# Performance work log

Measured on AMD Instinct MI355X. Metric: run time of the kernel, lower is better.

Reference implementation:

```python
import jax, jax.numpy as jnp
import numpy as np

N, E, G = 50000, 800000, 64
IN_NODE, OUT_NODE, IN_EDGE = 16, 20, 16
HID_E, N_ACT, HID_C = 64, 8, 256
BN_EPS = 1e-5


def setup_inputs() -> dict:
    key = jax.random.key(0)
    ks = jax.random.split(key, 12)
    def w(i, shape, scale=0.05):
        return jax.random.normal(ks[i], shape, jnp.float32) * scale
    return {
        "x": jax.random.normal(ks[0], (N, IN_NODE), jnp.float32),
        "edge_attr": jax.random.normal(ks[1], (E, IN_EDGE), jnp.float32),
        "a": jax.random.normal(ks[2], (G, N_ACT), jnp.float32),
        "edge_index": jax.random.randint(ks[3], (2, E), 0, N),
        "batch": jnp.sort(jax.random.randint(ks[4], (N,), 0, G)),
        # edge-conditioning MLP: Lin(16,64) -> BN(64) -> ReLU -> Lin(64, 16*20)
        "W1": w(5, (IN_EDGE, HID_E)), "b1": jnp.zeros((HID_E,), jnp.float32),
        "gamma": jnp.ones((HID_E,), jnp.float32), "beta": jnp.zeros((HID_E,), jnp.float32),
        "W2": w(6, (HID_E, IN_NODE * OUT_NODE)), "b2": jnp.zeros((IN_NODE * OUT_NODE,), jnp.float32),
        # NNConv root weight + bias
        "root_w": w(7, (IN_NODE, OUT_NODE)), "bias": jnp.zeros((OUT_NODE,), jnp.float32),
        # critic head: Lin(20+8,256) -> ReLU -> Lin(256,1)
        "Wc1": w(8, (OUT_NODE + N_ACT, HID_C)), "bc1": jnp.zeros((HID_C,), jnp.float32),
        "Wc2": w(9, (HID_C, 1)), "bc2": jnp.zeros((1,), jnp.float32),
    }


def reference(x, edge_attr, a, W1, b1, gamma, beta, W2, b2, root_w, bias,
              Wc1, bc1, Wc2, bc2, edge_index, batch):
    # edge-conditioning MLP (BatchNorm in training mode: batch stats over edges)
    h = edge_attr @ W1 + b1                              # [E, 64]
    mu = jnp.mean(h, axis=0)
    var = jnp.mean(jnp.square(h - mu), axis=0)           # biased var, as BN fwd
    h = (h - mu) * jax.lax.rsqrt(var + BN_EPS) * gamma + beta
    h = jax.nn.relu(h)
    w_e = (h @ W2 + b2).reshape(E, IN_NODE, OUT_NODE)    # per-edge weight matrix

    src, dst = edge_index[0], edge_index[1]
    msg = jnp.einsum('ei,eio->eo', x[src], w_e)          # gather + per-edge matvec [E, 20]
    aggr = jax.ops.segment_sum(msg, dst, num_segments=N) # scatter-add (NNConv aggr='add')
    out = x @ root_w + aggr + bias                       # [N, 20]

    # global mean pool over graphs
    sums = jax.ops.segment_sum(out, batch, num_segments=G)            # [G, 20]
    cnt = jax.ops.segment_sum(jnp.ones((N, 1), out.dtype), batch, num_segments=G)
    pooled = sums / jnp.maximum(cnt, 1.0)

    z = jnp.concatenate([pooled, a], axis=1)             # [G, 28]
    z = jax.nn.relu(z @ Wc1 + bc1)
    return z @ Wc2 + bc2                                 # [G, 1]
```

## Files before the change

### kernel.cpp

```cpp
#include <hip/hip_runtime.h>


#define E_EDGES   800000
#define N_NODES   50000
#define G_GRAPHS  64
#define EDGE_GRID 3072
#define NGROUPS   50000
#define GSTRIDE   768
#define NSUP      256
#define STAT_GRID 512
#define QSCALE    131072.0f
#define QINV      (1.0f / 131072.0f)

typedef _Float16 f16x2 __attribute__((ext_vector_type(2)));
typedef _Float16 f16x8 __attribute__((ext_vector_type(8)));
typedef __fp16   fp16x2 __attribute__((ext_vector_type(2)));
typedef float    f32x4 __attribute__((ext_vector_type(4)));
typedef unsigned u32x4 __attribute__((ext_vector_type(4)));

union H2U { f16x2 h; unsigned u; };
union F8U { f16x8 v; f16x2 h2[4]; u32x4 u4; };

__device__ __forceinline__ f16x2 pkrtz(float a, float b) {
  fp16x2 r = __builtin_amdgcn_cvt_pkrtz(a, b);
  return __builtin_bit_cast(f16x2, r);
}

__global__ __launch_bounds__(256) void setup_kernel(
    const float* __restrict__ W2, const float* __restrict__ b2,
    const float* __restrict__ W1, const float* __restrict__ x,
    const float* __restrict__ ea, unsigned* __restrict__ Bbuf,
    unsigned* __restrict__ Bw1, unsigned* __restrict__ xh,
    float* __restrict__ gstatsT)
{
  __shared__ float red[4][272];
  const int b = blockIdx.x, tid = threadIdx.x;
  if (b < STAT_GRID) {
    int lane = tid & 63, wave = tid >> 6;
    int nl = lane & 15, q = lane >> 4;
    int gw = b * 4 + wave;
    f32x4 acc = (f32x4){0.f, 0.f, 0.f, 0.f};
    float ms = 0.f;
    for (int c0 = gw; c0 < E_EDGES / 32; c0 += STAT_GRID * 4) {
      const float* p = ea + (size_t)(c0 * 32 + q * 8) * 16 + nl;
      float v0 = p[0],  v1 = p[16], v2 = p[32], v3 = p[48];
      float v4 = p[64], v5 = p[80], v6 = p[96], v7 = p[112];
      ms += (v0 + v1) + (v2 + v3) + (v4 + v5) + (v6 + v7);
      F8U av;
      av.h2[0] = pkrtz(v0, v1); av.h2[1] = pkrtz(v2, v3);
      av.h2[2] = pkrtz(v4, v5); av.h2[3] = pkrtz(v6, v7);
      acc = __builtin_amdgcn_mfma_f32_16x16x32_f16(av.v, av.v, acc, 0, 0, 0);
    }
    ms += __shfl_xor(ms, 16, 64);
    ms += __shfl_xor(ms, 32, 64);
#pragma unroll
    for (int r = 0; r < 4; ++r) red[wave][(q * 4 + r) * 16 + nl] = acc[r];
    if (q == 0) red[wave][256 + nl] = ms;
    __syncthreads();
    for (int v = tid; v < 272; v += 256)
      gstatsT[(size_t)v * STAT_GRID + b] =
          red[0][v] + red[1][v] + red[2][v] + red[3][v];
  } else if (b < STAT_GRID + 70) {
    int idx = (b - STAT_GRID) * 256 + tid;
    if (idx < 33 * 512) {
      int r = idx & 3, lane = (idx >> 2) & 63, nt = (idx >> 8) & 1,
          s = idx >> 9;
      int q = lane >> 4, nl = lane & 15, n = nt * 16 + nl;
      float v0 = 0.f, v1 = 0.f;
      if (n < 20) {
        if (s < 32) {
          int K0 = s * 32 + q * 8 + 2 * r;
          v0 = W2[(K0 >> 4) * 320 + (K0 & 15) * 20 + n];
          v1 = W2[((K0 + 1) >> 4) * 320 + ((K0 + 1) & 15) * 20 + n];
        } else if (q < 2) {
          int i0 = q * 8 + 2 * r;
          v0 = b2[i0 * 20 + n];
          v1 = b2[(i0 + 1) * 20 + n];
        }
      }
      H2U pk; pk.h = pkrtz(v0, v1);
      Bbuf[idx] = pk.u;
    } else {
      int idx2 = idx - 33 * 512;
      int r = idx2 & 3, lane = (idx2 >> 2) & 63, nt = idx2 >> 8;
      int q = lane >> 4, nl = lane & 15, n = nt * 16 + nl;
      int k0 = q * 8 + 2 * r;
      float v0 = (k0 < 16)     ? W1[k0 * 64 + n]       : 0.f;
      float v1 = (k0 + 1 < 16) ? W1[(k0 + 1) * 64 + n] : 0.f;
      H2U pk; pk.h = pkrtz(v0, v1);
      Bw1[idx2] = pk.u;
    }
  } else {
    int i = (b - STAT_GRID - 70) * 256 + tid;
    if (i < N_NODES * 8) {
      H2U pk; pk.h = pkrtz(x[2 * i], x[2 * i + 1]);
      xh[i] = pk.u;
    }
  }
}

__global__ __launch_bounds__(256) void mid_kernel(
    const float* __restrict__ gstatsT, const float* __restrict__ W1,
    const float* __restrict__ b1, const float* __restrict__ gamma,
    const float* __restrict__ beta, const float* __restrict__ x,
    const int* __restrict__ batch, float* __restrict__ sc,
    float* __restrict__ sh, float* __restrict__ sumx,
    float* __restrict__ cntf)
{
  const int t = threadIdx.x;
  if (blockIdx.x == G_GRAPHS) {
    __shared__ float S[272];
    for (int v = t; v < 272; v += 256) {
      const float* p = gstatsT + (size_t)v * STAT_GRID;
      float s = 0.f;
      for (int bb = 0; bb < STAT_GRID; ++bb) s += p[bb];
      S[v] = s;
    }
    __syncthreads();
    if (t < 64) {
      float w[16];
#pragma unroll
      for (int j = 0; j < 16; ++j) w[j] = W1[j * 64 + t];
      const float invE = 1.0f / (float)E_EDGES;
      float mw = 0.f;
#pragma unroll
      for (int j = 0; j < 16; ++j) mw += S[256 + j] * w[j];
      mw *= invE;
      float qf = 0.f;
      for (int j = 0; j < 16; ++j) {
        float tt = 0.f;
#pragma unroll
        for (int j2 = 0; j2 < 16; ++j2) tt += S[j * 16 + j2] * w[j2];
        qf += w[j] * tt;
      }
      qf *= invE;
      float b = b1[t];
      float meanH = mw + b;
      float eh2 = qf + 2.f * b * mw + b * b;
      float var = eh2 - meanH * meanH;
      float s = gamma[t] * rsqrtf(var + 1e-5f);
      sc[t] = s;
      sh[t] = beta[t] + (b - meanH) * s;
    }
  } else {
    int g = blockIdx.x;
    __shared__ int se[2];
    if (t < 2) {
      int key = g + t;
      int lo = 0, hi = N_NODES;
      while (lo < hi) {
        int mid = (lo + hi) >> 1;
        if (batch[mid] < key) lo = mid + 1; else hi = mid;
      }
      se[t] = lo;
    }
    __syncthreads();
    int start = se[0], end = se[1];
    int c = t & 15, rr = t >> 4;
    float s = 0.f;
    for (int n = start + rr; n < end; n += 16) s += x[(size_t)n * 16 + c];
    __shared__ float red[256];
    red[t] = s;
    __syncthreads();
#pragma unroll
    for (int st = 128; st >= 16; st >>= 1) {
      if (t < st) red[t] += red[t + st];
      __syncthreads();
    }
    if (t < 16) sumx[g * 16 + t] = red[t];
    if (t == 0) cntf[g] = (float)(end - start);
  }
}

__global__ __launch_bounds__(64, 3) void edge_kernel(
    const unsigned* __restrict__ xh, const float* __restrict__ ea,
    const int* __restrict__ ei, const int* __restrict__ batch,
    const float* __restrict__ sc, const float* __restrict__ sh,
    const unsigned* __restrict__ Bbuf, const unsigned* __restrict__ Bw1v,
    int* __restrict__ gpartI)
{
  __shared__ unsigned hh[320];
  __shared__ int gacc[1280];
  const int lane = threadIdx.x;
  const int nl = lane & 15, q = lane >> 4;
  const int s = blockIdx.x;
  const int kq = (s >> 3) & 3;
  const int sgroup = ((s >> 5) << 3) | (s & 7);
  const int* srcp = ei;
  const int* dstp = ei + E_EDGES;

  for (int v = lane; v < 1280; v += 64) gacc[v] = 0;

  F8U bb[8][2];
#pragma unroll
  for (int sl = 0; sl < 8; ++sl)
#pragma unroll
    for (int nt = 0; nt < 2; ++nt)
      bb[sl][nt].u4 =
          ((const u32x4*)Bbuf)[((kq * 8 + sl) * 2 + nt) * 64 + lane];
  F8U bx[2];
  if (kq == 3) {
    bx[0].u4 = ((const u32x4*)Bbuf)[64 * 64 + lane];
    bx[1].u4 = ((const u32x4*)Bbuf)[65 * 64 + lane];
  } else {
    bx[0].u4 = (u32x4){0u, 0u, 0u, 0u};
    bx[1].u4 = (u32x4){0u, 0u, 0u, 0u};
  }
  F8U bw1; bw1.u4 = ((const u32x4*)Bw1v)[kq * 64 + lane];
  const float scv = sc[kq * 16 + nl];
  const float shv = sh[kq * 16 + nl];
  const int hrb = (q >> 1) * 20 + nl;
  const int qh = q & 1;

  int g = sgroup;
  f32x4 eaA = (f32x4){0.f,0.f,0.f,0.f}, eaB = eaA;
  u32x4 xp = (u32x4){0u,0u,0u,0u};
  int gq0 = 0, gq1 = 0, gq2 = 0, gq3 = 0;
  {
    int base = g * 16;
    if (q < 2) {
      const float* p = ea + (size_t)(base + nl) * 16 + q * 8;
      eaA = *(const f32x4*)p;
      eaB = *(const f32x4*)(p + 4);
    }
    int src = srcp[base + nl];
    xp = ((const u32x4*)xh)[src * 2 + qh];
    gq0 = batch[dstp[base + q * 4 + 0]];
    gq1 = batch[dstp[base + q * 4 + 1]];
    gq2 = batch[dstp[base + q * 4 + 2]];
    gq3 = batch[dstp[base + q * 4 + 3]];
  }

  while (g < NGROUPS) {
    const int gn = g + GSTRIDE;

    {
      F8U aEA;
      if (q < 2) {
        aEA.h2[0] = pkrtz(eaA[0], eaA[1]); aEA.h2[1] = pkrtz(eaA[2], eaA[3]);
        aEA.h2[2] = pkrtz(eaB[0], eaB[1]); aEA.h2[3] = pkrtz(eaB[2], eaB[3]);
      } else {
        aEA.u4 = (u32x4){0u, 0u, 0u, 0u};
      }
      f32x4 hD = __builtin_amdgcn_mfma_f32_16x16x32_f16(
          aEA.v, bw1.v, (f32x4){0.f, 0.f, 0.f, 0.f}, 0, 0, 0);
#pragma unroll
      for (int r = 0; r < 4; ++r) {
        float h = fmaxf(hD[r] * scv + shv, 0.f);
        H2U pk; pk.h = pkrtz(h, h);
        hh[nl * 20 + q * 4 + r] = pk.u;
      }
    }
    F8U xcur; xcur.u4 = xp;

    f32x4 eaAn = (f32x4){0.f,0.f,0.f,0.f}, eaBn = eaAn;
    u32x4 xpn = (u32x4){0u,0u,0u,0u};
    int gq0n = 0, gq1n = 0, gq2n = 0, gq3n = 0;
    if (gn < NGROUPS) {
      int base = gn * 16;
      if (q < 2) {
        const float* p = ea + (size_t)(base + nl) * 16 + q * 8;
        eaAn = *(const f32x4*)p;
        eaBn = *(const f32x4*)(p + 4);
      }
      int src = srcp[base + nl];
      xpn = ((const u32x4*)xh)[src * 2 + qh];
      gq0n = batch[dstp[base + q * 4 + 0]];
      gq1n = batch[dstp[base + q * 4 + 1]];
      gq2n = batch[dstp[base + q * 4 + 2]];
      gq3n = batch[dstp[base + q * 4 + 3]];
    }

    f32x4 acc0 = (f32x4){0.f, 0.f, 0.f, 0.f};
    f32x4 acc1 = (f32x4){0.f, 0.f, 0.f, 0.f};
#pragma unroll
    for (int sl = 0; sl < 8; ++sl) {
      H2U hu; hu.u = hh[hrb + sl * 40];
      F8U av;
      av.h2[0] = hu.h * xcur.h2[0];
      av.h2[1] = hu.h * xcur.h2[1];
      av.h2[2] = hu.h * xcur.h2[2];
      av.h2[3] = hu.h * xcur.h2[3];
      acc0 = __builtin_amdgcn_mfma_f32_16x16x32_f16(av.v, bb[sl][0].v, acc0,
                                                    0, 0, 0);
      acc1 = __builtin_amdgcn_mfma_f32_16x16x32_f16(av.v, bb[sl][1].v, acc1,
                                                    0, 0, 0);
    }
    if (kq == 3) {
      F8U av;
      if (q < 2) av = xcur;
      else       av.u4 = (u32x4){0u, 0u, 0u, 0u};
      acc0 = __builtin_amdgcn_mfma_f32_16x16x32_f16(av.v, bx[0].v, acc0,
                                                    0, 0, 0);
      acc1 = __builtin_amdgcn_mfma_f32_16x16x32_f16(av.v, bx[1].v, acc1,
                                                    0, 0, 0);
    }

    {
      int gi;
      gi = gq0 * 20;
      atomicAdd(&gacc[gi + nl], __float2int_rn(acc0[0] * QSCALE));
      if (nl < 4) atomicAdd(&gacc[gi + 16 + nl], __float2int_rn(acc1[0] * QSCALE));
      gi = gq1 * 20;
      atomicAdd(&gacc[gi + nl], __float2int_rn(acc0[1] * QSCALE));
      if (nl < 4) atomicAdd(&gacc[gi + 16 + nl], __float2int_rn(acc1[1] * QSCALE));
      gi = gq2 * 20;
      atomicAdd(&gacc[gi + nl], __float2int_rn(acc0[2] * QSCALE));
      if (nl < 4) atomicAdd(&gacc[gi + 16 + nl], __float2int_rn(acc1[2] * QSCALE));
      gi = gq3 * 20;
      atomicAdd(&gacc[gi + nl], __float2int_rn(acc0[3] * QSCALE));
      if (nl < 4) atomicAdd(&gacc[gi + 16 + nl], __float2int_rn(acc1[3] * QSCALE));
    }

    g = gn;
    eaA = eaAn; eaB = eaBn; xp = xpn;
    gq0 = gq0n; gq1 = gq1n; gq2 = gq2n; gq3 = gq3n;
  }

  const int ssup = s & (NSUP - 1);
  for (int v = lane; v < 1280; v += 64) {
    int gg = v / 20, o = v - gg * 20;
    atomicAdd(&gpartI[(gg * NSUP + ssup) * 20 + o], gacc[v]);
  }
}

__global__ __launch_bounds__(256) void critic_kernel(
    const int* __restrict__ gpartI, const float* __restrict__ sumx,
    const float* __restrict__ cntf, const float* __restrict__ root_w,
    const float* __restrict__ bias, const float* __restrict__ a,
    const float* __restrict__ Wc1, const float* __restrict__ bc1,
    const float* __restrict__ Wc2, const float* __restrict__ bc2,
    float* __restrict__ out)
{
  int g = blockIdx.x, t = threadIdx.x;
  __shared__ int part[240];
  __shared__ float pooled[20];
  if (t < 240) {
    int col = t % 20, r = t / 20;
    int s = 0;
    const int* gp = gpartI + (size_t)g * NSUP * 20;
    for (int sl = r; sl < NSUP; sl += 12) s += gp[sl * 20 + col];
    part[t] = s;
  }
  __syncthreads();
  if (t < 20) {
    int si = 0;
#pragma unroll
    for (int r = 0; r < 12; ++r) si += part[r * 20 + t];
    float s = (float)si * QINV;
    float cnt = cntf[g];
    float base = bias[t] * cnt;
#pragma unroll
    for (int i = 0; i < 16; ++i) base += sumx[g * 16 + i] * root_w[i * 20 + t];
    pooled[t] = (s + base) / fmaxf(cnt, 1.f);
  }
  __syncthreads();
  float z = bc1[t];
#pragma unroll
  for (int j = 0; j < 20; ++j) z += pooled[j] * Wc1[j * 256 + t];
#pragma unroll
  for (int j = 0; j < 8; ++j) z += a[g * 8 + j] * Wc1[(20 + j) * 256 + t];
  z = fmaxf(z, 0.f);
  float pr = z * Wc2[t];
#pragma unroll
  for (int off = 32; off >= 1; off >>= 1) pr += __shfl_down(pr, off, 64);
  __shared__ float red[4];
  if ((t & 63) == 0) red[t >> 6] = pr;
  __syncthreads();
  if (t == 0) out[g] = red[0] + red[1] + red[2] + red[3] + bc2[0];
}

extern "C" void kernel_launch(void* const* d_in, const int* in_sizes, int n_in,
                              void* d_out, int out_size, void* d_ws,
                              size_t ws_size, hipStream_t stream) {
  const float* x         = (const float*)d_in[0];
  const float* edge_attr = (const float*)d_in[1];
  const float* a         = (const float*)d_in[2];
  const int*   ei        = (const int*)d_in[3];
  const int*   batch     = (const int*)d_in[4];
  const float* W1        = (const float*)d_in[5];
  const float* b1        = (const float*)d_in[6];
  const float* gamma     = (const float*)d_in[7];
  const float* beta      = (const float*)d_in[8];
  const float* W2        = (const float*)d_in[9];
  const float* b2        = (const float*)d_in[10];
  const float* root_w    = (const float*)d_in[11];
  const float* bias      = (const float*)d_in[12];
  const float* Wc1       = (const float*)d_in[13];
  const float* bc1       = (const float*)d_in[14];
  const float* Wc2       = (const float*)d_in[15];
  const float* bc2       = (const float*)d_in[16];
  float* out = (float*)d_out;

  float* wsf     = (float*)d_ws;
  float* sc      = wsf;
  float* sh      = wsf + 64;
  float* sumx    = wsf + 128;
  float* cntf    = wsf + 1152;
  unsigned* Bw1  = (unsigned*)(wsf + 1216);
  unsigned* Bbuf = (unsigned*)(wsf + 2240);
  float* gstatsT = wsf + 19136;
  unsigned* xhp  = (unsigned*)(wsf + 158400);
  int* gpartI    = (int*)(wsf + 558400);

  (void)hipMemsetAsync(gpartI, 0, (size_t)G_GRAPHS * NSUP * 20 * sizeof(int),
                       stream);

  const int XCONV_BLOCKS = (N_NODES * 8 + 255) / 256;
  setup_kernel<<<STAT_GRID + 70 + XCONV_BLOCKS, 256, 0, stream>>>(
      W2, b2, W1, x, edge_attr, Bbuf, Bw1, xhp, gstatsT);
  mid_kernel<<<G_GRAPHS + 1, 256, 0, stream>>>(gstatsT, W1, b1, gamma, beta,
                                               x, batch, sc, sh, sumx, cntf);
  edge_kernel<<<EDGE_GRID, 64, 0, stream>>>(xhp, edge_attr, ei, batch, sc,
                                            sh, Bbuf, Bw1, gpartI);
  critic_kernel<<<G_GRAPHS, 256, 0, stream>>>(gpartI, sumx, cntf, root_w,
                                              bias, a, Wc1, bc1, Wc2, bc2,
                                              out);
}
```

Measured before the change: 251.4 us.

## Run two waves per edge block sharing LDS accumulators, shuffle graph ids

The edge kernel moves from one wave per block to two waves per block, keeping the same block count, so total waves double and the group stride goes to 1536. The two waves share one LDS per-graph accumulator, which halves per-wave LDS flushes to global memory. Each lane now loads one batch id per edge, and the four per-row ids are fetched with wave shuffles instead of four redundant gathers. The BN stats reduction also gets four independent accumulators for more memory-level parallelism. The trade-off is extra barriers and more LDS atomic contention within a block.

```diff
diff --git a/kernel.cpp b/kernel.cpp
--- a/kernel.cpp
+++ b/kernel.cpp
@@ -4,9 +4,9 @@
 #define E_EDGES   800000
 #define N_NODES   50000
 #define G_GRAPHS  64
-#define EDGE_GRID 3072
+#define EDGE_BLOCKS 3072
 #define NGROUPS   50000
-#define GSTRIDE   768
+#define GSTRIDE   1536
 #define NSUP      256
 #define STAT_GRID 512
 #define QSCALE    131072.0f
@@ -112,9 +112,11 @@
     __shared__ float S[272];
     for (int v = t; v < 272; v += 256) {
       const float* p = gstatsT + (size_t)v * STAT_GRID;
-      float s = 0.f;
-      for (int bb = 0; bb < STAT_GRID; ++bb) s += p[bb];
-      S[v] = s;
+      float s0 = 0.f, s1 = 0.f, s2 = 0.f, s3 = 0.f;
+      for (int bb = 0; bb < STAT_GRID; bb += 4) {
+        s0 += p[bb]; s1 += p[bb + 1]; s2 += p[bb + 2]; s3 += p[bb + 3];
+      }
+      S[v] = (s0 + s1) + (s2 + s3);
     }
     __syncthreads();
     if (t < 64) {
@@ -172,24 +174,25 @@
   }
 }
 
-__global__ __launch_bounds__(64, 3) void edge_kernel(
+__global__ __launch_bounds__(128, 6) void edge_kernel(
     const unsigned* __restrict__ xh, const float* __restrict__ ea,
     const int* __restrict__ ei, const int* __restrict__ batch,
     const float* __restrict__ sc, const float* __restrict__ sh,
     const unsigned* __restrict__ Bbuf, const unsigned* __restrict__ Bw1v,
     int* __restrict__ gpartI)
 {
-  __shared__ unsigned hh[320];
+  __shared__ unsigned hh[2][320];
   __shared__ int gacc[1280];
-  const int lane = threadIdx.x;
+  const int tid = threadIdx.x;
+  const int lane = tid & 63, wv = tid >> 6;
   const int nl = lane & 15, q = lane >> 4;
-  const int s = blockIdx.x;
-  const int kq = (s >> 3) & 3;
-  const int sgroup = ((s >> 5) << 3) | (s & 7);
+  const int ws = blockIdx.x * 2 + wv;
+  const int kq = (ws >> 4) & 3;
+  const int sgroup = ((ws >> 6) << 4) | (ws & 15);
   const int* srcp = ei;
   const int* dstp = ei + E_EDGES;
 
-  for (int v = lane; v < 1280; v += 64) gacc[v] = 0;
+  for (int v = tid; v < 1280; v += 128) gacc[v] = 0;
 
   F8U bb[8][2];
 #pragma unroll
@@ -209,13 +212,15 @@
   F8U bw1; bw1.u4 = ((const u32x4*)Bw1v)[kq * 64 + lane];
   const float scv = sc[kq * 16 + nl];
   const float shv = sh[kq * 16 + nl];
+  unsigned* myhh = hh[wv];
   const int hrb = (q >> 1) * 20 + nl;
   const int qh = q & 1;
+  __syncthreads();
 
   int g = sgroup;
   f32x4 eaA = (f32x4){0.f,0.f,0.f,0.f}, eaB = eaA;
   u32x4 xp = (u32x4){0u,0u,0u,0u};
-  int gq0 = 0, gq1 = 0, gq2 = 0, gq3 = 0;
+  int ge = 0;
   {
     int base = g * 16;
     if (q < 2) {
@@ -225,10 +230,7 @@
     }
     int src = srcp[base + nl];
     xp = ((const u32x4*)xh)[src * 2 + qh];
-    gq0 = batch[dstp[base + q * 4 + 0]];
-    gq1 = batch[dstp[base + q * 4 + 1]];
-    gq2 = batch[dstp[base + q * 4 + 2]];
-    gq3 = batch[dstp[base + q * 4 + 3]];
+    ge = batch[dstp[base + nl]];
   }
 
   while (g < NGROUPS) {
@@ -248,14 +250,18 @@
       for (int r = 0; r < 4; ++r) {
         float h = fmaxf(hD[r] * scv + shv, 0.f);
         H2U pk; pk.h = pkrtz(h, h);
-        hh[nl * 20 + q * 4 + r] = pk.u;
+        myhh[nl * 20 + q * 4 + r] = pk.u;
       }
     }
     F8U xcur; xcur.u4 = xp;
+    int gq0 = __shfl(ge, q * 4 + 0, 64);
+    int gq1 = __shfl(ge, q * 4 + 1, 64);
+    int gq2 = __shfl(ge, q * 4 + 2, 64);
+    int gq3 = __shfl(ge, q * 4 + 3, 64);
 
     f32x4 eaAn = (f32x4){0.f,0.f,0.f,0.f}, eaBn = eaAn;
     u32x4 xpn = (u32x4){0u,0u,0u,0u};
-    int gq0n = 0, gq1n = 0, gq2n = 0, gq3n = 0;
+    int gen = 0;
     if (gn < NGROUPS) {
       int base = gn * 16;
       if (q < 2) {
@@ -265,17 +271,14 @@
       }
       int src = srcp[base + nl];
       xpn = ((const u32x4*)xh)[src * 2 + qh];
-      gq0n = batch[dstp[base + q * 4 + 0]];
-      gq1n = batch[dstp[base + q * 4 + 1]];
-      gq2n = batch[dstp[base + q * 4 + 2]];
-      gq3n = batch[dstp[base + q * 4 + 3]];
+      gen = batch[dstp[base + nl]];
     }
 
     f32x4 acc0 = (f32x4){0.f, 0.f, 0.f, 0.f};
     f32x4 acc1 = (f32x4){0.f, 0.f, 0.f, 0.f};
 #pragma unroll
     for (int sl = 0; sl < 8; ++sl) {
-      H2U hu; hu.u = hh[hrb + sl * 40];
+      H2U hu; hu.u = myhh[hrb + sl * 40];
       F8U av;
       av.h2[0] = hu.h * xcur.h2[0];
       av.h2[1] = hu.h * xcur.h2[1];
@@ -313,12 +316,12 @@
     }
 
     g = gn;
-    eaA = eaAn; eaB = eaBn; xp = xpn;
-    gq0 = gq0n; gq1 = gq1n; gq2 = gq2n; gq3 = gq3n;
-  }
-
-  const int ssup = s & (NSUP - 1);
-  for (int v = lane; v < 1280; v += 64) {
+    eaA = eaAn; eaB = eaBn; xp = xpn; ge = gen;
+  }
+
+  __syncthreads();
+  const int ssup = blockIdx.x & (NSUP - 1);
+  for (int v = tid; v < 1280; v += 128) {
     int gg = v / 20, o = v - gg * 20;
     atomicAdd(&gpartI[(gg * NSUP + ssup) * 20 + o], gacc[v]);
   }
@@ -411,8 +414,8 @@
       W2, b2, W1, x, edge_attr, Bbuf, Bw1, xhp, gstatsT);
   mid_kernel<<<G_GRAPHS + 1, 256, 0, stream>>>(gstatsT, W1, b1, gamma, beta,
                                                x, batch, sc, sh, sumx, cntf);
-  edge_kernel<<<EDGE_GRID, 64, 0, stream>>>(xhp, edge_attr, ei, batch, sc,
-                                            sh, Bbuf, Bw1, gpartI);
+  edge_kernel<<<EDGE_BLOCKS, 128, 0, stream>>>(xhp, edge_attr, ei, batch, sc,
+                                               sh, Bbuf, Bw1, gpartI);
   critic_kernel<<<G_GRAPHS, 256, 0, stream>>>(gpartI, sumx, cntf, root_w,
                                               bias, a, Wc1, bc1, Wc2, bc2,
                                               out);
```

Result: slower. 531.8 us (+111.5%).
